# Kernel optimization log

Measured on AMD Instinct MI355X. Metric: run time of the kernel, lower is better.

The kernel has to match this reference:

```python
import jax, jax.numpy as jnp
import numpy as np

HEAD_DIM = 64
CLIP = 64  # clipping_distance
B, S = 32, 1024


def setup_inputs() -> dict:
    key = jax.random.key(0)
    kq, kk, kv, km, kt = jax.random.split(key, 5)
    q = jax.random.normal(kq, (B, S, HEAD_DIM), dtype=jnp.float32)
    k = jax.random.normal(kk, (B, S, HEAD_DIM), dtype=jnp.float32)
    v = jax.random.normal(kv, (B, S, HEAD_DIM), dtype=jnp.float32)
    mask = jax.random.randint(km, (B, S, S), 0, 2).astype(jnp.bool_)
    pos_table = jax.random.normal(kt, (2 * CLIP + 1, HEAD_DIM), dtype=jnp.float32)
    return {"q": q, "k": k, "v": v, "mask": mask, "pos_table": pos_table}


def reference(q, k, v, mask, pos_table):
    scaling = 1.0 / np.sqrt(HEAD_DIM).astype(np.float32)
    Sq, Sk = q.shape[1], k.shape[1]
    # relative positions k_idx - q_idx, clipped to [-CLIP, CLIP]
    rel = jnp.arange(Sk)[None, :] - jnp.arange(Sq)[:, None]      # [Sq, Sk]
    idx = jnp.clip(rel, -CLIP, CLIP) + CLIP                      # [Sq, Sk]
    pe = pos_table[idx]                                          # [Sq, Sk, D]
    # content logits + relative positional logits
    logits = jnp.einsum('bqd,bkd->bqk', q, k) + jnp.einsum('bqd,qkd->bqk', q, pe)
    logits = logits * scaling
    logits = jnp.where(mask, -jnp.inf, logits)
    attn = jax.nn.softmax(logits, axis=-1)                       # [B, Sq, Sk]
    return jnp.einsum('bqk,bkd->bqd', attn, v)
```

## Files before the change

kernel.cpp:

```cpp
#include <hip/hip_runtime.h>
#include <stdint.h>

#define BATCH 32
#define SEQ   1024
#define DIM   64
#define NKT   (SEQ / 64)

typedef uint16_t u16;
typedef uint32_t u32;
typedef __attribute__((ext_vector_type(8))) __bf16 bf16x8;
typedef __attribute__((ext_vector_type(4))) float  f32x4;
typedef __attribute__((ext_vector_type(4))) u32    u32x4;

__device__ __forceinline__ u16 f2bf(float f) {
    u32 x = __builtin_bit_cast(u32, f);
    x += 0x7FFFu + ((x >> 16) & 1u);
    return (u16)(x >> 16);
}

__device__ __forceinline__ bf16x8 cvt8(const float* __restrict__ p) {
    f32x4 a = *reinterpret_cast<const f32x4*>(p);
    f32x4 b = *reinterpret_cast<const f32x4*>(p + 4);
    u16 t[8];
    t[0] = f2bf(a[0]); t[1] = f2bf(a[1]); t[2] = f2bf(a[2]); t[3] = f2bf(a[3]);
    t[4] = f2bf(b[0]); t[5] = f2bf(b[1]); t[6] = f2bf(b[2]); t[7] = f2bf(b[3]);
    return __builtin_bit_cast(bf16x8, *reinterpret_cast<u32x4*>(t));
}

__device__ __forceinline__ bf16x8 ldg8(const u16* p) {
    u32x4 u = *reinterpret_cast<const u32x4*>(p);
    return __builtin_bit_cast(bf16x8, u);
}

__global__ __launch_bounds__(256) void vt_kernel(const float* __restrict__ v,
                                                 u16* __restrict__ vt) {
    __shared__ u16 tile[64][72];
    const int b  = blockIdx.y;
    const int k0 = blockIdx.x * 64;
    const int t  = threadIdx.x;
    const float* vb  = v  + (size_t)b * SEQ * DIM;
    u16*         vtb = vt + (size_t)b * DIM * SEQ;

    {
        int kk = t >> 2;
        int d0 = (t & 3) * 16;
        const float* src = vb + (size_t)(k0 + kk) * DIM + d0;
        u16 tmp[16];
#pragma unroll
        for (int i = 0; i < 4; ++i) {
            f32x4 a = *reinterpret_cast<const f32x4*>(src + i * 4);
            tmp[i * 4 + 0] = f2bf(a[0]); tmp[i * 4 + 1] = f2bf(a[1]);
            tmp[i * 4 + 2] = f2bf(a[2]); tmp[i * 4 + 3] = f2bf(a[3]);
        }
        *reinterpret_cast<u32x4*>(&tile[kk][d0])     = *reinterpret_cast<u32x4*>(tmp);
        *reinterpret_cast<u32x4*>(&tile[kk][d0 + 8]) = *reinterpret_cast<u32x4*>(tmp + 8);
    }
    __syncthreads();
#pragma unroll
    for (int i = 0; i < 2; ++i) {
        int d  = t / 8 + i * 32;
        int ks = (t % 8) * 8;
        u16 tmp[8];
#pragma unroll
        for (int j = 0; j < 8; ++j) tmp[j] = tile[ks + j][d];
        *reinterpret_cast<u32x4*>(vtb + (size_t)d * SEQ + k0 + ks) =
            *reinterpret_cast<u32x4*>(tmp);
    }
}

template <bool USE_VT>
__global__ __launch_bounds__(256, 2) void attn_kernel(
    const float* __restrict__ qg, const float* __restrict__ kg,
    const void* __restrict__ vgv, const int* __restrict__ maskg,
    const float* __restrict__ ptg, float* __restrict__ outg) {
    __shared__ float qp[64][132];
    __shared__ int   mlds[4][16][68];
    __shared__ u16   plds[4][16][72];

    const int b    = blockIdx.y;
    const int q0   = blockIdx.x * 64;
    const int tid  = threadIdx.x;
    const int wave = tid >> 6;
    const int lane = tid & 63;
    const int quad = lane >> 4;
    const int c16  = lane & 15;

    const float* qb = qg + ((size_t)b * SEQ + q0) * DIM;
    const float* kb = kg + (size_t)b * SEQ * DIM;
    const int*   mb = maskg + ((size_t)b * SEQ + q0) * SEQ;

    const bf16x8 qA0 = cvt8(qb + (size_t)(wave * 16 + c16) * DIM + quad * 8);
    const bf16x8 qA1 = cvt8(qb + (size_t)(wave * 16 + c16) * DIM + 32 + quad * 8);

    for (int jt = 0; jt < 9; ++jt) {
        int j0 = jt * 16;
        int jr = min(j0 + c16, 128);
        bf16x8 b0 = cvt8(ptg + (size_t)jr * DIM + quad * 8);
        bf16x8 b1 = cvt8(ptg + (size_t)jr * DIM + 32 + quad * 8);
        f32x4 acc = {0.f, 0.f, 0.f, 0.f};
        acc = __builtin_amdgcn_mfma_f32_16x16x32_bf16(qA0, b0, acc, 0, 0, 0);
        acc = __builtin_amdgcn_mfma_f32_16x16x32_bf16(qA1, b1, acc, 0, 0, 0);
        int jcol = j0 + c16;
        if (jcol <= 128) {
#pragma unroll
            for (int r = 0; r < 4; ++r)
                qp[wave * 16 + quad * 4 + r][jcol] = acc[r];
        }
    }

    float m_run[4], l_run[4];
    f32x4 O[4];
#pragma unroll
    for (int r = 0; r < 4; ++r) { m_run[r] = -1e30f; l_run[r] = 0.f; }
#pragma unroll
    for (int d = 0; d < 4; ++d) O[d] = f32x4{0.f, 0.f, 0.f, 0.f};

#pragma unroll 1
    for (int kt = 0; kt < NKT; ++kt) {
        const int k0 = kt * 64;

        {
            int row_l = lane >> 2;
            const int* mrow = mb + (size_t)(wave * 16 + row_l) * SEQ + k0;
#pragma unroll
            for (int i = 0; i < 4; ++i) {
                int seg = (lane & 3) + i * 4;
                *reinterpret_cast<u32x4*>(&mlds[wave][row_l][seg * 4]) =
                    *reinterpret_cast<const u32x4*>(mrow + seg * 4);
            }
        }

        f32x4 S[4];
#pragma unroll
        for (int sub = 0; sub < 4; ++sub) {
            const float* kr = kb + (size_t)(k0 + sub * 16 + c16) * DIM;
            bf16x8 kb0 = cvt8(kr + quad * 8);
            bf16x8 kb1 = cvt8(kr + 32 + quad * 8);
            f32x4 acc = {0.f, 0.f, 0.f, 0.f};
            acc = __builtin_amdgcn_mfma_f32_16x16x32_bf16(qA0, kb0, acc, 0, 0, 0);
            acc = __builtin_amdgcn_mfma_f32_16x16x32_bf16(qA1, kb1, acc, 0, 0, 0);
            S[sub] = acc;
        }

        float sv[4][4];
#pragma unroll
        for (int sub = 0; sub < 4; ++sub) {
#pragma unroll
            for (int r = 0; r < 4; ++r) {
                int row_l = quad * 4 + r;
                int row_g = q0 + wave * 16 + row_l;
                int col_g = k0 + sub * 16 + c16;
                int rel = col_g - row_g;
                rel = rel < -64 ? -64 : (rel > 64 ? 64 : rel);
                float x = (S[sub][r] + qp[wave * 16 + row_l][rel + 64]) * 0.125f;
                int mv = mlds[wave][row_l][sub * 16 + c16];
                sv[sub][r] = mv ? -1e30f : x;
            }
        }

        float m_new[4], alpha[4];
#pragma unroll
        for (int r = 0; r < 4; ++r) {
            float rmax = fmaxf(fmaxf(sv[0][r], sv[1][r]), fmaxf(sv[2][r], sv[3][r]));
            rmax = fmaxf(rmax, __shfl_xor(rmax, 1));
            rmax = fmaxf(rmax, __shfl_xor(rmax, 2));
            rmax = fmaxf(rmax, __shfl_xor(rmax, 4));
            rmax = fmaxf(rmax, __shfl_xor(rmax, 8));
            m_new[r] = fmaxf(m_run[r], rmax);
            alpha[r] = __expf(m_run[r] - m_new[r]);
            m_run[r] = m_new[r];
        }
#pragma unroll
        for (int r = 0; r < 4; ++r) {
            float rs = 0.f;
#pragma unroll
            for (int sub = 0; sub < 4; ++sub) {
                float e = __expf(sv[sub][r] - m_new[r]);
                rs += e;
                plds[wave][quad * 4 + r][sub * 16 + c16] = f2bf(e);
            }
            rs += __shfl_xor(rs, 1);
            rs += __shfl_xor(rs, 2);
            rs += __shfl_xor(rs, 4);
            rs += __shfl_xor(rs, 8);
            l_run[r] = l_run[r] * alpha[r] + rs;
#pragma unroll
            for (int d = 0; d < 4; ++d) O[d][r] *= alpha[r];
        }

        bf16x8 pA0 = *reinterpret_cast<bf16x8*>(&plds[wave][c16][quad * 8]);
        bf16x8 pA1 = *reinterpret_cast<bf16x8*>(&plds[wave][c16][32 + quad * 8]);
#pragma unroll
        for (int d = 0; d < 4; ++d) {
            bf16x8 vb0, vb1;
            if (USE_VT) {
                const u16* vtb = (const u16*)vgv + (size_t)b * DIM * SEQ +
                                 (size_t)(d * 16 + c16) * SEQ + k0;
                vb0 = ldg8(vtb + quad * 8);
                vb1 = ldg8(vtb + 32 + quad * 8);
            } else {
                u16 t0[8], t1[8];
                const float* vbase = (const float*)vgv +
                                     ((size_t)b * SEQ + k0) * DIM + d * 16 + c16;
#pragma unroll
                for (int j = 0; j < 8; ++j) {
                    t0[j] = f2bf(vbase[(size_t)(quad * 8 + j) * DIM]);
                    t1[j] = f2bf(vbase[(size_t)(32 + quad * 8 + j) * DIM]);
                }
                vb0 = __builtin_bit_cast(bf16x8, *reinterpret_cast<u32x4*>(t0));
                vb1 = __builtin_bit_cast(bf16x8, *reinterpret_cast<u32x4*>(t1));
            }
            O[d] = __builtin_amdgcn_mfma_f32_16x16x32_bf16(pA0, vb0, O[d], 0, 0, 0);
            O[d] = __builtin_amdgcn_mfma_f32_16x16x32_bf16(pA1, vb1, O[d], 0, 0, 0);
        }
    }

    float* ob = outg + ((size_t)b * SEQ + q0) * DIM;
#pragma unroll
    for (int r = 0; r < 4; ++r) {
        float inv = 1.f / l_run[r];
        int row_l = wave * 16 + quad * 4 + r;
#pragma unroll
        for (int d = 0; d < 4; ++d)
            ob[(size_t)row_l * DIM + d * 16 + c16] = O[d][r] * inv;
    }
}

extern "C" void kernel_launch(void* const* d_in, const int* in_sizes, int n_in,
                              void* d_out, int out_size, void* d_ws, size_t ws_size,
                              hipStream_t stream) {
    const float* q    = (const float*)d_in[0];
    const float* k    = (const float*)d_in[1];
    const float* v    = (const float*)d_in[2];
    const int*   mask = (const int*)d_in[3];
    const float* pt   = (const float*)d_in[4];
    float* out        = (float*)d_out;

    const size_t vt_bytes = (size_t)BATCH * SEQ * DIM * sizeof(u16);
    dim3 grid(SEQ / 64, BATCH);

    if (ws_size >= vt_bytes) {
        u16* vt = (u16*)d_ws;
        vt_kernel<<<grid, 256, 0, stream>>>(v, vt);
        attn_kernel<true><<<grid, 256, 0, stream>>>(q, k, (const void*)vt, mask, pt, out);
    } else {
        attn_kernel<false><<<grid, 256, 0, stream>>>(q, k, (const void*)v, mask, pt, out);
    }
}
```

Before: 274.8 us.

## Pre-convert inputs to bf16, bit-pack mask, drop online max in attention

New measurement: 291.3 us. 6.0% more time.

```diff
diff --git a/kernel.cpp b/kernel.cpp
--- a/kernel.cpp
+++ b/kernel.cpp
@@ -5,31 +5,60 @@
 #define SEQ   1024
 #define DIM   64
 #define NKT   (SEQ / 64)
+#define SCALE_LOG2E 0.180336879f
 
 typedef uint16_t u16;
 typedef uint32_t u32;
+typedef unsigned long long u64;
 typedef __attribute__((ext_vector_type(8))) __bf16 bf16x8;
 typedef __attribute__((ext_vector_type(4))) float  f32x4;
 typedef __attribute__((ext_vector_type(4))) u32    u32x4;
+typedef __attribute__((ext_vector_type(2))) u32    u32x2;
 
 __device__ __forceinline__ u16 f2bf(float f) {
     u32 x = __builtin_bit_cast(u32, f);
     x += 0x7FFFu + ((x >> 16) & 1u);
     return (u16)(x >> 16);
 }
-
+__device__ __forceinline__ bf16x8 ldg8(const u16* p) {
+    u32x4 u = *reinterpret_cast<const u32x4*>(p);
+    return __builtin_bit_cast(bf16x8, u);
+}
 __device__ __forceinline__ bf16x8 cvt8(const float* __restrict__ p) {
     f32x4 a = *reinterpret_cast<const f32x4*>(p);
     f32x4 b = *reinterpret_cast<const f32x4*>(p + 4);
     u16 t[8];
-    t[0] = f2bf(a[0]); t[1] = f2bf(a[1]); t[2] = f2bf(a[2]); t[3] = f2bf(a[3]);
-    t[4] = f2bf(b[0]); t[5] = f2bf(b[1]); t[6] = f2bf(b[2]); t[7] = f2bf(b[3]);
+    t[0]=f2bf(a[0]); t[1]=f2bf(a[1]); t[2]=f2bf(a[2]); t[3]=f2bf(a[3]);
+    t[4]=f2bf(b[0]); t[5]=f2bf(b[1]); t[6]=f2bf(b[2]); t[7]=f2bf(b[3]);
     return __builtin_bit_cast(bf16x8, *reinterpret_cast<u32x4*>(t));
 }
 
-__device__ __forceinline__ bf16x8 ldg8(const u16* p) {
-    u32x4 u = *reinterpret_cast<const u32x4*>(p);
-    return __builtin_bit_cast(bf16x8, u);
+__global__ __launch_bounds__(256) void pack_mask(const int* __restrict__ m,
+                                                 u64* __restrict__ pm) {
+    const int lane = threadIdx.x & 63;
+    const int wid  = (blockIdx.x * 256 + (int)threadIdx.x) >> 6;
+    const int w0   = wid * 128;
+#pragma unroll 2
+    for (int it = 0; it < 32; ++it) {
+        int wb = w0 + it * 4;
+        const int* p = m + (size_t)wb * 64 + lane;
+        int x0 = p[0], x1 = p[64], x2 = p[128], x3 = p[192];
+        u64 b0 = __ballot(x0 != 0);
+        u64 b1 = __ballot(x1 != 0);
+        u64 b2 = __ballot(x2 != 0);
+        u64 b3 = __ballot(x3 != 0);
+        if (lane == 0) { pm[wb]=b0; pm[wb+1]=b1; pm[wb+2]=b2; pm[wb+3]=b3; }
+    }
+}
+
+__global__ __launch_bounds__(256) void cvt_bf16(const float* __restrict__ src,
+                                                u16* __restrict__ dst,
+                                                int n4, float scale) {
+    int i = blockIdx.x * 256 + threadIdx.x;
+    if (i >= n4) return;
+    f32x4 a = *reinterpret_cast<const f32x4*>(src + (size_t)i * 4);
+    u16 t[4] = { f2bf(a[0]*scale), f2bf(a[1]*scale), f2bf(a[2]*scale), f2bf(a[3]*scale) };
+    *reinterpret_cast<u32x2*>(dst + (size_t)i * 4) = *reinterpret_cast<u32x2*>(t);
 }
 
 __global__ __launch_bounds__(256) void vt_kernel(const float* __restrict__ v,
@@ -40,17 +69,15 @@
     const int t  = threadIdx.x;
     const float* vb  = v  + (size_t)b * SEQ * DIM;
     u16*         vtb = vt + (size_t)b * DIM * SEQ;
-
     {
-        int kk = t >> 2;
-        int d0 = (t & 3) * 16;
+        int kk = t >> 2, d0 = (t & 3) * 16;
         const float* src = vb + (size_t)(k0 + kk) * DIM + d0;
         u16 tmp[16];
 #pragma unroll
         for (int i = 0; i < 4; ++i) {
             f32x4 a = *reinterpret_cast<const f32x4*>(src + i * 4);
-            tmp[i * 4 + 0] = f2bf(a[0]); tmp[i * 4 + 1] = f2bf(a[1]);
-            tmp[i * 4 + 2] = f2bf(a[2]); tmp[i * 4 + 3] = f2bf(a[3]);
+            tmp[i*4+0]=f2bf(a[0]); tmp[i*4+1]=f2bf(a[1]);
+            tmp[i*4+2]=f2bf(a[2]); tmp[i*4+3]=f2bf(a[3]);
         }
         *reinterpret_cast<u32x4*>(&tile[kk][d0])     = *reinterpret_cast<u32x4*>(tmp);
         *reinterpret_cast<u32x4*>(&tile[kk][d0 + 8]) = *reinterpret_cast<u32x4*>(tmp + 8);
@@ -68,105 +95,229 @@
     }
 }
 
-template <bool USE_VT>
-__global__ __launch_bounds__(256, 2) void attn_kernel(
+__global__ __launch_bounds__(128) void attn2(
+    const u16* __restrict__ qb, const u16* __restrict__ kb,
+    const u16* __restrict__ vt, const u64* __restrict__ pm,
+    const u16* __restrict__ ptb, float* __restrict__ outg) {
+    __shared__ float qp[2][16][132];
+    __shared__ u16   plds[2][16][72];
+
+    const int b    = blockIdx.y;
+    const int q0   = blockIdx.x * 32;
+    const int wave = threadIdx.x >> 6;
+    const int lane = threadIdx.x & 63;
+    const int quad = lane >> 4;
+    const int c16  = lane & 15;
+    const int rw0  = q0 + wave * 16;
+
+    const u16* qrow = qb + ((size_t)b * SEQ + rw0 + c16) * DIM;
+    const bf16x8 qA0 = ldg8(qrow + quad * 8);
+    const bf16x8 qA1 = ldg8(qrow + 32 + quad * 8);
+
+    for (int jt = 0; jt < 9; ++jt) {
+        int jr = min(jt * 16 + c16, 128);
+        const u16* pr = ptb + (size_t)jr * DIM;
+        bf16x8 b0 = ldg8(pr + quad * 8);
+        bf16x8 b1 = ldg8(pr + 32 + quad * 8);
+        f32x4 acc = {0.f, 0.f, 0.f, 0.f};
+        acc = __builtin_amdgcn_mfma_f32_16x16x32_bf16(qA0, b0, acc, 0, 0, 0);
+        acc = __builtin_amdgcn_mfma_f32_16x16x32_bf16(qA1, b1, acc, 0, 0, 0);
+        int jc = jt * 16 + c16;
+        if (jc <= 128) {
+#pragma unroll
+            for (int r = 0; r < 4; ++r) qp[wave][quad * 4 + r][jc] = acc[r];
+        }
+    }
+
+    const u16* kbb = kb + (size_t)b * SEQ * DIM;
+    const u16* vtb = vt + (size_t)b * DIM * SEQ;
+    const u64* pmb = pm + ((size_t)b * SEQ + rw0) * 16;
+
+    bf16x8 kcur[8];
+    u32 mlo[4], mhi[4];
+#pragma unroll
+    for (int sub = 0; sub < 4; ++sub) {
+        const u16* base = kbb + (size_t)(sub * 16 + c16) * DIM;
+        kcur[2*sub]   = ldg8(base + quad * 8);
+        kcur[2*sub+1] = ldg8(base + 32 + quad * 8);
+    }
+#pragma unroll
+    for (int r = 0; r < 4; ++r) {
+        u64 w = pmb[(size_t)(quad * 4 + r) * 16];
+        mlo[r] = (u32)w; mhi[r] = (u32)(w >> 32);
+    }
+
+    float lrun[4] = {0.f, 0.f, 0.f, 0.f};
+    f32x4 O[4];
+#pragma unroll
+    for (int d = 0; d < 4; ++d) O[d] = f32x4{0.f, 0.f, 0.f, 0.f};
+
+#pragma unroll 1
+    for (int kt = 0; kt < NKT; ++kt) {
+        const int k0 = kt * 64;
+
+        bf16x8 vf[8];
+#pragma unroll
+        for (int d = 0; d < 4; ++d) {
+            const u16* vbase = vtb + (size_t)(d * 16 + c16) * SEQ + k0;
+            vf[2*d]   = ldg8(vbase + quad * 8);
+            vf[2*d+1] = ldg8(vbase + 32 + quad * 8);
+        }
+        bf16x8 kn[8];
+        u32 nlo[4], nhi[4];
+        {
+            int ktn = (kt < NKT - 1) ? kt + 1 : kt;
+            int kn0 = ktn * 64;
+#pragma unroll
+            for (int sub = 0; sub < 4; ++sub) {
+                const u16* base = kbb + (size_t)(kn0 + sub * 16 + c16) * DIM;
+                kn[2*sub]   = ldg8(base + quad * 8);
+                kn[2*sub+1] = ldg8(base + 32 + quad * 8);
+            }
+#pragma unroll
+            for (int r = 0; r < 4; ++r) {
+                u64 w = pmb[(size_t)(quad * 4 + r) * 16 + ktn];
+                nlo[r] = (u32)w; nhi[r] = (u32)(w >> 32);
+            }
+        }
+
+        f32x4 S[4];
+#pragma unroll
+        for (int sub = 0; sub < 4; ++sub) {
+            f32x4 acc = {0.f, 0.f, 0.f, 0.f};
+            acc = __builtin_amdgcn_mfma_f32_16x16x32_bf16(qA0, kcur[2*sub],   acc, 0, 0, 0);
+            acc = __builtin_amdgcn_mfma_f32_16x16x32_bf16(qA1, kcur[2*sub+1], acc, 0, 0, 0);
+            S[sub] = acc;
+        }
+
+#pragma unroll
+        for (int r = 0; r < 4; ++r) {
+            int row_l = quad * 4 + r;
+            int row_g = rw0 + row_l;
+#pragma unroll
+            for (int sub = 0; sub < 4; ++sub) {
+                int col = k0 + sub * 16 + c16;
+                int rel = col - row_g;
+                rel = rel < -64 ? -64 : (rel > 64 ? 64 : rel);
+                float x = S[sub][r] + qp[wave][row_l][rel + 64];
+                float e = exp2f(x);
+                u32 mb = (sub & 2) ? mhi[r] : mlo[r];
+                u32 bit = (mb >> ((sub & 1) * 16 + c16)) & 1u;
+                e = bit ? 0.f : e;
+                lrun[r] += e;
+                plds[wave][row_l][sub * 16 + c16] = f2bf(e);
+            }
+        }
+
+        bf16x8 pA0 = *reinterpret_cast<bf16x8*>(&plds[wave][c16][quad * 8]);
+        bf16x8 pA1 = *reinterpret_cast<bf16x8*>(&plds[wave][c16][32 + quad * 8]);
+#pragma unroll
+        for (int d = 0; d < 4; ++d) {
+            O[d] = __builtin_amdgcn_mfma_f32_16x16x32_bf16(pA0, vf[2*d],   O[d], 0, 0, 0);
+            O[d] = __builtin_amdgcn_mfma_f32_16x16x32_bf16(pA1, vf[2*d+1], O[d], 0, 0, 0);
+        }
+#pragma unroll
+        for (int i = 0; i < 8; ++i) kcur[i] = kn[i];
+#pragma unroll
+        for (int r = 0; r < 4; ++r) { mlo[r] = nlo[r]; mhi[r] = nhi[r]; }
+    }
+
+    float* ob = outg + ((size_t)b * SEQ + rw0) * DIM;
+#pragma unroll
+    for (int r = 0; r < 4; ++r) {
+        float l = lrun[r];
+        l += __shfl_xor(l, 1);
+        l += __shfl_xor(l, 2);
+        l += __shfl_xor(l, 4);
+        l += __shfl_xor(l, 8);
+        float inv = 1.f / l;
+        int row_l = quad * 4 + r;
+#pragma unroll
+        for (int d = 0; d < 4; ++d)
+            ob[(size_t)row_l * DIM + d * 16 + c16] = O[d][r] * inv;
+    }
+}
+
+__global__ __launch_bounds__(256, 2) void attn_fb(
     const float* __restrict__ qg, const float* __restrict__ kg,
-    const void* __restrict__ vgv, const int* __restrict__ maskg,
+    const float* __restrict__ vg, const int* __restrict__ maskg,
     const float* __restrict__ ptg, float* __restrict__ outg) {
     __shared__ float qp[64][132];
     __shared__ int   mlds[4][16][68];
     __shared__ u16   plds[4][16][72];
 
-    const int b    = blockIdx.y;
-    const int q0   = blockIdx.x * 64;
-    const int tid  = threadIdx.x;
-    const int wave = tid >> 6;
-    const int lane = tid & 63;
-    const int quad = lane >> 4;
-    const int c16  = lane & 15;
-
-    const float* qb = qg + ((size_t)b * SEQ + q0) * DIM;
-    const float* kb = kg + (size_t)b * SEQ * DIM;
-    const int*   mb = maskg + ((size_t)b * SEQ + q0) * SEQ;
-
-    const bf16x8 qA0 = cvt8(qb + (size_t)(wave * 16 + c16) * DIM + quad * 8);
-    const bf16x8 qA1 = cvt8(qb + (size_t)(wave * 16 + c16) * DIM + 32 + quad * 8);
+    const int b = blockIdx.y, q0 = blockIdx.x * 64;
+    const int tid = threadIdx.x, wave = tid >> 6, lane = tid & 63;
+    const int quad = lane >> 4, c16 = lane & 15;
+
+    const float* qb2 = qg + ((size_t)b * SEQ + q0) * DIM;
+    const float* kb2 = kg + (size_t)b * SEQ * DIM;
+    const int*   mb  = maskg + ((size_t)b * SEQ + q0) * SEQ;
+
+    const bf16x8 qA0 = cvt8(qb2 + (size_t)(wave*16 + c16) * DIM + quad * 8);
+    const bf16x8 qA1 = cvt8(qb2 + (size_t)(wave*16 + c16) * DIM + 32 + quad * 8);
 
     for (int jt = 0; jt < 9; ++jt) {
-        int j0 = jt * 16;
-        int jr = min(j0 + c16, 128);
+        int jr = min(jt * 16 + c16, 128);
         bf16x8 b0 = cvt8(ptg + (size_t)jr * DIM + quad * 8);
         bf16x8 b1 = cvt8(ptg + (size_t)jr * DIM + 32 + quad * 8);
-        f32x4 acc = {0.f, 0.f, 0.f, 0.f};
-        acc = __builtin_amdgcn_mfma_f32_16x16x32_bf16(qA0, b0, acc, 0, 0, 0);
-        acc = __builtin_amdgcn_mfma_f32_16x16x32_bf16(qA1, b1, acc, 0, 0, 0);
-        int jcol = j0 + c16;
-        if (jcol <= 128) {
-#pragma unroll
-            for (int r = 0; r < 4; ++r)
-                qp[wave * 16 + quad * 4 + r][jcol] = acc[r];
-        }
-    }
-
+        f32x4 acc = {0.f,0.f,0.f,0.f};
+        acc = __builtin_amdgcn_mfma_f32_16x16x32_bf16(qA0, b0, acc, 0,0,0);
+        acc = __builtin_amdgcn_mfma_f32_16x16x32_bf16(qA1, b1, acc, 0,0,0);
+        int jc = jt * 16 + c16;
+        if (jc <= 128) {
+#pragma unroll
+            for (int r = 0; r < 4; ++r) qp[wave*16 + quad*4 + r][jc] = acc[r];
+        }
+    }
     float m_run[4], l_run[4];
     f32x4 O[4];
 #pragma unroll
     for (int r = 0; r < 4; ++r) { m_run[r] = -1e30f; l_run[r] = 0.f; }
 #pragma unroll
-    for (int d = 0; d < 4; ++d) O[d] = f32x4{0.f, 0.f, 0.f, 0.f};
+    for (int d = 0; d < 4; ++d) O[d] = f32x4{0.f,0.f,0.f,0.f};
 
 #pragma unroll 1
     for (int kt = 0; kt < NKT; ++kt) {
         const int k0 = kt * 64;
-
         {
             int row_l = lane >> 2;
-            const int* mrow = mb + (size_t)(wave * 16 + row_l) * SEQ + k0;
+            const int* mrow = mb + (size_t)(wave*16 + row_l) * SEQ + k0;
 #pragma unroll
             for (int i = 0; i < 4; ++i) {
                 int seg = (lane & 3) + i * 4;
-                *reinterpret_cast<u32x4*>(&mlds[wave][row_l][seg * 4]) =
-                    *reinterpret_cast<const u32x4*>(mrow + seg * 4);
-            }
-        }
-
+                *reinterpret_cast<u32x4*>(&mlds[wave][row_l][seg*4]) =
+                    *reinterpret_cast<const u32x4*>(mrow + seg*4);
+            }
+        }
         f32x4 S[4];
 #pragma unroll
         for (int sub = 0; sub < 4; ++sub) {
-            const float* kr = kb + (size_t)(k0 + sub * 16 + c16) * DIM;
-            bf16x8 kb0 = cvt8(kr + quad * 8);
-            bf16x8 kb1 = cvt8(kr + 32 + quad * 8);
-            f32x4 acc = {0.f, 0.f, 0.f, 0.f};
-            acc = __builtin_amdgcn_mfma_f32_16x16x32_bf16(qA0, kb0, acc, 0, 0, 0);
-            acc = __builtin_amdgcn_mfma_f32_16x16x32_bf16(qA1, kb1, acc, 0, 0, 0);
+            const float* kr = kb2 + (size_t)(k0 + sub*16 + c16) * DIM;
+            bf16x8 kb0 = cvt8(kr + quad*8), kb1 = cvt8(kr + 32 + quad*8);
+            f32x4 acc = {0.f,0.f,0.f,0.f};
+            acc = __builtin_amdgcn_mfma_f32_16x16x32_bf16(qA0, kb0, acc, 0,0,0);
+            acc = __builtin_amdgcn_mfma_f32_16x16x32_bf16(qA1, kb1, acc, 0,0,0);
             S[sub] = acc;
         }
-
         float sv[4][4];
 #pragma unroll
-        for (int sub = 0; sub < 4; ++sub) {
+        for (int sub = 0; sub < 4; ++sub)
 #pragma unroll
             for (int r = 0; r < 4; ++r) {
-                int row_l = quad * 4 + r;
-                int row_g = q0 + wave * 16 + row_l;
-                int col_g = k0 + sub * 16 + c16;
-                int rel = col_g - row_g;
-                rel = rel < -64 ? -64 : (rel > 64 ? 64 : rel);
-                float x = (S[sub][r] + qp[wave * 16 + row_l][rel + 64]) * 0.125f;
-                int mv = mlds[wave][row_l][sub * 16 + c16];
-                sv[sub][r] = mv ? -1e30f : x;
-            }
-        }
-
+                int row_l = quad*4 + r, row_g = q0 + wave*16 + row_l;
+                int col = k0 + sub*16 + c16;
+                int rel = col - row_g; rel = rel < -64 ? -64 : (rel > 64 ? 64 : rel);
+                float x = (S[sub][r] + qp[wave*16 + row_l][rel + 64]) * 0.125f;
+                sv[sub][r] = mlds[wave][row_l][sub*16 + c16] ? -1e30f : x;
+            }
         float m_new[4], alpha[4];
 #pragma unroll
         for (int r = 0; r < 4; ++r) {
-            float rmax = fmaxf(fmaxf(sv[0][r], sv[1][r]), fmaxf(sv[2][r], sv[3][r]));
-            rmax = fmaxf(rmax, __shfl_xor(rmax, 1));
-            rmax = fmaxf(rmax, __shfl_xor(rmax, 2));
-            rmax = fmaxf(rmax, __shfl_xor(rmax, 4));
-            rmax = fmaxf(rmax, __shfl_xor(rmax, 8));
-            m_new[r] = fmaxf(m_run[r], rmax);
+            float rm = fmaxf(fmaxf(sv[0][r], sv[1][r]), fmaxf(sv[2][r], sv[3][r]));
+            rm = fmaxf(rm, __shfl_xor(rm, 1)); rm = fmaxf(rm, __shfl_xor(rm, 2));
+            rm = fmaxf(rm, __shfl_xor(rm, 4)); rm = fmaxf(rm, __shfl_xor(rm, 8));
+            m_new[r] = fmaxf(m_run[r], rm);
             alpha[r] = __expf(m_run[r] - m_new[r]);
             m_run[r] = m_new[r];
         }
@@ -177,52 +328,39 @@
             for (int sub = 0; sub < 4; ++sub) {
                 float e = __expf(sv[sub][r] - m_new[r]);
                 rs += e;
-                plds[wave][quad * 4 + r][sub * 16 + c16] = f2bf(e);
-            }
-            rs += __shfl_xor(rs, 1);
-            rs += __shfl_xor(rs, 2);
-            rs += __shfl_xor(rs, 4);
-            rs += __shfl_xor(rs, 8);
+                plds[wave][quad*4 + r][sub*16 + c16] = f2bf(e);
+            }
+            rs += __shfl_xor(rs, 1); rs += __shfl_xor(rs, 2);
+            rs += __shfl_xor(rs, 4); rs += __shfl_xor(rs, 8);
             l_run[r] = l_run[r] * alpha[r] + rs;
 #pragma unroll
             for (int d = 0; d < 4; ++d) O[d][r] *= alpha[r];
         }
-
-        bf16x8 pA0 = *reinterpret_cast<bf16x8*>(&plds[wave][c16][quad * 8]);
-        bf16x8 pA1 = *reinterpret_cast<bf16x8*>(&plds[wave][c16][32 + quad * 8]);
+        bf16x8 pA0 = *reinterpret_cast<bf16x8*>(&plds[wave][c16][quad*8]);
+        bf16x8 pA1 = *reinterpret_cast<bf16x8*>(&plds[wave][c16][32 + quad*8]);
 #pragma unroll
         for (int d = 0; d < 4; ++d) {
-            bf16x8 vb0, vb1;
-            if (USE_VT) {
-                const u16* vtb = (const u16*)vgv + (size_t)b * DIM * SEQ +
-                                 (size_t)(d * 16 + c16) * SEQ + k0;
-                vb0 = ldg8(vtb + quad * 8);
-                vb1 = ldg8(vtb + 32 + quad * 8);
-            } else {
-                u16 t0[8], t1[8];
-                const float* vbase = (const float*)vgv +
-                                     ((size_t)b * SEQ + k0) * DIM + d * 16 + c16;
-#pragma unroll
-                for (int j = 0; j < 8; ++j) {
-                    t0[j] = f2bf(vbase[(size_t)(quad * 8 + j) * DIM]);
-                    t1[j] = f2bf(vbase[(size_t)(32 + quad * 8 + j) * DIM]);
-                }
-                vb0 = __builtin_bit_cast(bf16x8, *reinterpret_cast<u32x4*>(t0));
-                vb1 = __builtin_bit_cast(bf16x8, *reinterpret_cast<u32x4*>(t1));
-            }
-            O[d] = __builtin_amdgcn_mfma_f32_16x16x32_bf16(pA0, vb0, O[d], 0, 0, 0);
-            O[d] = __builtin_amdgcn_mfma_f32_16x16x32_bf16(pA1, vb1, O[d], 0, 0, 0);
-        }
-    }
-
+            u16 t0[8], t1[8];
+            const float* vb2 = vg + ((size_t)b * SEQ + k0) * DIM + d*16 + c16;
+#pragma unroll
+            for (int j = 0; j < 8; ++j) {
+                t0[j] = f2bf(vb2[(size_t)(quad*8 + j) * DIM]);
+                t1[j] = f2bf(vb2[(size_t)(32 + quad*8 + j) * DIM]);
+            }
+            bf16x8 vb0 = __builtin_bit_cast(bf16x8, *reinterpret_cast<u32x4*>(t0));
+            bf16x8 vb1 = __builtin_bit_cast(bf16x8, *reinterpret_cast<u32x4*>(t1));
+            O[d] = __builtin_amdgcn_mfma_f32_16x16x32_bf16(pA0, vb0, O[d], 0,0,0);
+            O[d] = __builtin_amdgcn_mfma_f32_16x16x32_bf16(pA1, vb1, O[d], 0,0,0);
+        }
+    }
     float* ob = outg + ((size_t)b * SEQ + q0) * DIM;
 #pragma unroll
     for (int r = 0; r < 4; ++r) {
         float inv = 1.f / l_run[r];
-        int row_l = wave * 16 + quad * 4 + r;
+        int row_l = wave*16 + quad*4 + r;
 #pragma unroll
         for (int d = 0; d < 4; ++d)
-            ob[(size_t)row_l * DIM + d * 16 + c16] = O[d][r] * inv;
+            ob[(size_t)row_l * DIM + d*16 + c16] = O[d][r] * inv;
     }
 }
 
@@ -236,14 +374,27 @@
     const float* pt   = (const float*)d_in[4];
     float* out        = (float*)d_out;
 
-    const size_t vt_bytes = (size_t)BATCH * SEQ * DIM * sizeof(u16);
-    dim3 grid(SEQ / 64, BATCH);
-
-    if (ws_size >= vt_bytes) {
-        u16* vt = (u16*)d_ws;
-        vt_kernel<<<grid, 256, 0, stream>>>(v, vt);
-        attn_kernel<true><<<grid, 256, 0, stream>>>(q, k, (const void*)vt, mask, pt, out);
+    const size_t PM_B = (size_t)BATCH * SEQ * (SEQ / 64) * 8;
+    const size_t VT_B = (size_t)BATCH * SEQ * DIM * 2;
+    const size_t QB_B = VT_B, KB_B = VT_B;
+    const size_t PT_B = 32768;
+    const size_t need = PM_B + VT_B + QB_B + KB_B + PT_B;
+
+    if (ws_size >= need) {
+        char* w = (char*)d_ws;
+        u64* pmp = (u64*)w;  w += PM_B;
+        u16* vtp = (u16*)w;  w += VT_B;
+        u16* qbp = (u16*)w;  w += QB_B;
+        u16* kbp = (u16*)w;  w += KB_B;
+        u16* ptp = (u16*)w;
+
+        pack_mask<<<1024, 256, 0, stream>>>(mask, pmp);
+        cvt_bf16<<<2048, 256, 0, stream>>>(q, qbp, 524288, SCALE_LOG2E);
+        cvt_bf16<<<2048, 256, 0, stream>>>(k, kbp, 524288, 1.0f);
+        cvt_bf16<<<9,    256, 0, stream>>>(pt, ptp, 2064, 1.0f);
+        vt_kernel<<<dim3(SEQ / 64, BATCH), 256, 0, stream>>>(v, vtp);
+        attn2<<<dim3(SEQ / 32, BATCH), 128, 0, stream>>>(qbp, kbp, vtp, pmp, ptp, out);
     } else {
-        attn_kernel<false><<<grid, 256, 0, stream>>>(q, k, (const void*)v, mask, pt, out);
-    }
-}
+        attn_fb<<<dim3(SEQ / 64, BATCH), 256, 0, stream>>>(q, k, v, mask, pt, out);
+    }
+}
```
